# Kernel tuning notes

Hardware: AMD Instinct MI355X
Metric: run time of the kernel (lower is better)

Reference implementation:

```python
import jax, jax.numpy as jnp
import numpy as np

DIM = 768
NUM_EXPERTS = 1536
EXPERT_DIM = 64
NOISE_SCALE = 0.1
B, H, W = 1, 64, 64
N = B * H * W


def setup_inputs() -> dict:
    key = jax.random.key(0)
    ks = jax.random.split(key, 6)
    scaled = lambda k, shape, fan_in: (jax.random.normal(k, shape, jnp.float32) / np.sqrt(fan_in)).astype(jnp.float32)
    return {
        "x": jax.random.normal(ks[0], (B, H, W, DIM), jnp.float32),
        "noise": jax.random.normal(ks[1], (N, NUM_EXPERTS), jnp.float32),
        "gate_w": scaled(ks[2], (NUM_EXPERTS, DIM), DIM),
        "gate_b": jnp.zeros((NUM_EXPERTS,), jnp.float32),
        "expert_w": scaled(ks[3], (NUM_EXPERTS, EXPERT_DIM, DIM), DIM),  # torch Linear weight layout (out, in)
        "expert_b": jnp.zeros((NUM_EXPERTS, EXPERT_DIM), jnp.float32),
        "proj_w": scaled(ks[4], (DIM, EXPERT_DIM), EXPERT_DIM),
        "proj_b": jnp.zeros((DIM,), jnp.float32),
    }


def reference(x, noise, gate_w, gate_b, expert_w, expert_b, proj_w, proj_b):
    orig_shape = x.shape
    xf = x.reshape(-1, orig_shape[-1])  # (N, DIM)
    # Noisy gating
    scores = xf @ gate_w.T + gate_b + noise * NOISE_SCALE  # (N, E)
    gate_weights = jax.nn.softmax(scores, axis=-1)
    top_w, top_i = jax.lax.top_k(gate_weights, 1)  # (N, 1), (N, 1)
    idx = top_i[:, 0]  # (N,)
    # Gather only the selected expert per token (same math as the redundant
    # dense all-expert compute followed by a gather in the original).
    w_sel = expert_w[idx]  # (N, EXPERT_DIM, DIM)
    b_sel = expert_b[idx]  # (N, EXPERT_DIM)
    y = jnp.einsum('nd,nod->no', xf, w_sel) + b_sel  # (N, EXPERT_DIM)
    out_flat = (y @ proj_w.T + proj_b) * top_w  # (N, DIM); top_w broadcasts (N,1)
    return out_flat.reshape(orig_shape)
```

## Files before the change

### kernel.cpp

```cpp
#include <hip/hip_runtime.h>
#include <hip/hip_bf16.h>

#define NT 4096
#define DIM 768
#define NE 1536
#define ED 64
#define GAP_THR 8e-3f

typedef __attribute__((ext_vector_type(8))) short short8v;
typedef __attribute__((ext_vector_type(4))) float f32x4;

__device__ __forceinline__ unsigned short f2bf(float f) {
  unsigned int u = __float_as_uint(f);
  unsigned int r = (u + 0x7fffu + ((u >> 16) & 1u)) >> 16;
  return (unsigned short)r;
}
__device__ __forceinline__ float bf2f(unsigned short h) {
  return __uint_as_float(((unsigned int)h) << 16);
}

__device__ __forceinline__ void gload16(const void* g, void* l) {
  __builtin_amdgcn_global_load_lds((const __attribute__((address_space(1))) void*)g,
                                   (__attribute__((address_space(3))) void*)l, 16, 0, 0);
}

__device__ __forceinline__ void top2_merge(float& m1, int& i1, float& m2, int& i2,
                                           float om1, int oi1, float om2, int oi2) {
  if (om1 > m1 || (om1 == m1 && oi1 < i1)) {
    if (m1 > om2 || (m1 == om2 && i1 < oi2)) { m2 = m1; i2 = i1; }
    else { m2 = om2; i2 = oi2; }
    m1 = om1; i1 = oi1;
  } else {
    if (om1 > m2 || (om1 == m2 && oi1 < i2)) { m2 = om1; i2 = oi1; }
  }
}

__global__ __launch_bounds__(256) void split_all(
    const float* __restrict__ x, const float* __restrict__ gw,
    unsigned short* __restrict__ xhi, unsigned short* __restrict__ xlo,
    unsigned short* __restrict__ ghi, unsigned short* __restrict__ glo,
    int* __restrict__ rc_cnt) {
  if (blockIdx.x == 0 && threadIdx.x == 0) *rc_cnt = 0;
  const int nx4 = NT * DIM / 4;
  const int ng4 = NE * DIM / 4;
  int i = blockIdx.x * 256 + threadIdx.x;
  const float* src; unsigned short* hi; unsigned short* lo; int j;
  if (i < nx4) { src = x; hi = xhi; lo = xlo; j = i; }
  else { j = i - nx4; if (j >= ng4) return; src = gw; hi = ghi; lo = glo; }
  float4 v = ((const float4*)src)[j];
  unsigned short h0 = f2bf(v.x), h1 = f2bf(v.y), h2 = f2bf(v.z), h3 = f2bf(v.w);
  ((ushort4*)hi)[j] = make_ushort4(h0, h1, h2, h3);
  ((ushort4*)lo)[j] = make_ushort4(f2bf(v.x - bf2f(h0)), f2bf(v.y - bf2f(h1)),
                                   f2bf(v.z - bf2f(h2)), f2bf(v.w - bf2f(h3)));
}

__global__ __launch_bounds__(256) void gate_mfma(
    const unsigned short* __restrict__ xhi, const unsigned short* __restrict__ xlo,
    const unsigned short* __restrict__ ghi, const unsigned short* __restrict__ glo,
    const float* __restrict__ gb, const float* __restrict__ noise,
    float4* __restrict__ part_a, int* __restrict__ part_i2) {
  __shared__ __align__(16) unsigned short sA[2 * 128 * 32];
  __shared__ __align__(16) unsigned short sB[2 * 128 * 32];
  const int tid = threadIdx.x;
  const int w = tid >> 6, lane = tid & 63;
  const int wr = w >> 1, wc = w & 1;
  const int bm = blockIdx.x, bn = blockIdx.y;
  const int fr = lane & 15;
  const int fg = lane >> 4;
  const int gsw = fg ^ ((fr >> 1) & 3);

  f32x4 acc[4][4];
#pragma unroll
  for (int i = 0; i < 4; i++)
#pragma unroll
    for (int j = 0; j < 4; j++) acc[i][j] = (f32x4){0.f, 0.f, 0.f, 0.f};

  const size_t arow = (size_t)bm * 128 * DIM;
  const size_t brow = (size_t)bn * 128 * DIM;
  const int sr_lo = tid >> 2;
  const int sg = (tid & 3) ^ ((tid >> 3) & 3);

  for (int kt = 0; kt < DIM; kt += 32) {
    __syncthreads();
#pragma unroll
    for (int h = 0; h < 2; h++) {
      const int r = h * 64 + sr_lo;
      const size_t asrc = arow + (size_t)r * DIM + kt + sg * 8;
      const size_t bsrc = brow + (size_t)r * DIM + kt + sg * 8;
      const int dofs = h * 2048 + w * 512;
      gload16(xhi + asrc, &sA[dofs]);
      gload16(xlo + asrc, &sA[4096 + dofs]);
      gload16(ghi + bsrc, &sB[dofs]);
      gload16(glo + bsrc, &sB[4096 + dofs]);
    }
    __syncthreads();

    short8v ah[4], al[4], bh[4], bl[4];
#pragma unroll
    for (int mf = 0; mf < 4; mf++) {
      int ro = (wr * 64 + mf * 16 + fr) * 32 + gsw * 8;
      ah[mf] = *(const short8v*)&sA[ro];
      al[mf] = *(const short8v*)&sA[4096 + ro];
    }
#pragma unroll
    for (int nf = 0; nf < 4; nf++) {
      int ro = (wc * 64 + nf * 16 + fr) * 32 + gsw * 8;
      bh[nf] = *(const short8v*)&sB[ro];
      bl[nf] = *(const short8v*)&sB[4096 + ro];
    }
#pragma unroll
    for (int mf = 0; mf < 4; mf++)
#pragma unroll
      for (int nf = 0; nf < 4; nf++) {
        f32x4 c = acc[mf][nf];
        c = __builtin_amdgcn_mfma_f32_16x16x32_bf16(ah[mf], bh[nf], c, 0, 0, 0);
        c = __builtin_amdgcn_mfma_f32_16x16x32_bf16(ah[mf], bl[nf], c, 0, 0, 0);
        c = __builtin_amdgcn_mfma_f32_16x16x32_bf16(al[mf], bh[nf], c, 0, 0, 0);
        acc[mf][nf] = c;
      }
  }

  const int gm0 = bm * 128 + wr * 64;
  const int gn0 = bn * 128 + wc * 64;
  const int chunk = bn * 2 + wc;
  int gcol[4]; float gbv[4];
#pragma unroll
  for (int nf = 0; nf < 4; nf++) { gcol[nf] = gn0 + nf * 16 + fr; gbv[nf] = gb[gcol[nf]]; }
#pragma unroll
  for (int mf = 0; mf < 4; mf++) {
    float sv[4][4];
#pragma unroll
    for (int nf = 0; nf < 4; nf++)
#pragma unroll
      for (int reg = 0; reg < 4; reg++) {
        int gm = gm0 + mf * 16 + fg * 4 + reg;
        sv[nf][reg] = acc[mf][nf][reg] + gbv[nf] + 0.1f * noise[(size_t)gm * NE + gcol[nf]];
      }
#pragma unroll
    for (int reg = 0; reg < 4; reg++) {
      float m1 = sv[0][reg]; int i1 = gcol[0];
      float m2 = -3e38f; int i2 = 0x7fffffff;
#pragma unroll
      for (int nf = 1; nf < 4; nf++) {
        float v = sv[nf][reg]; int ii = gcol[nf];
        if (v > m1 || (v == m1 && ii < i1)) { m2 = m1; i2 = i1; m1 = v; i1 = ii; }
        else if (v > m2 || (v == m2 && ii < i2)) { m2 = v; i2 = ii; }
      }
#pragma unroll
      for (int off = 1; off <= 8; off <<= 1) {
        float om1 = __shfl_xor(m1, off, 64); int oi1 = __shfl_xor(i1, off, 64);
        float om2 = __shfl_xor(m2, off, 64); int oi2 = __shfl_xor(i2, off, 64);
        top2_merge(m1, i1, m2, i2, om1, oi1, om2, oi2);
      }
      float ssum = 0.f;
#pragma unroll
      for (int nf = 0; nf < 4; nf++) ssum += __expf(sv[nf][reg] - m1);
#pragma unroll
      for (int off = 1; off <= 8; off <<= 1) ssum += __shfl_xor(ssum, off, 64);
      if (fr == 0) {
        int gm = gm0 + mf * 16 + fg * 4 + reg;
        part_a[(size_t)gm * 24 + chunk] = make_float4(m1, m2, ssum, __int_as_float(i1));
        part_i2[(size_t)gm * 24 + chunk] = i2;
      }
    }
  }
}

__global__ __launch_bounds__(256) void finalize(
    const float4* __restrict__ part_a, const int* __restrict__ part_i2,
    float* __restrict__ topw, int* __restrict__ idx,
    int* __restrict__ rc_count, int* __restrict__ rc_n, int* __restrict__ rc_i2) {
  const int wv = threadIdx.x >> 6, lane = threadIdx.x & 63;
  const int n = blockIdx.x * 4 + wv;
  float m1 = -3e38f, m2 = -3e38f, lm1 = -3e38f, lsum = 0.f;
  int i1 = 0x7fffffff, i2 = 0x7fffffff;
  if (lane < 24) {
    float4 pa = part_a[(size_t)n * 24 + lane];
    m1 = pa.x; m2 = pa.y; lsum = pa.z; i1 = __float_as_int(pa.w);
    i2 = part_i2[(size_t)n * 24 + lane];
    lm1 = pa.x;
  }
#pragma unroll
  for (int off = 1; off <= 32; off <<= 1) {
    float om1 = __shfl_xor(m1, off, 64); int oi1 = __shfl_xor(i1, off, 64);
    float om2 = __shfl_xor(m2, off, 64); int oi2 = __shfl_xor(i2, off, 64);
    top2_merge(m1, i1, m2, i2, om1, oi1, om2, oi2);
  }
  float contrib = (lane < 24) ? __expf(lm1 - m1) * lsum : 0.f;
#pragma unroll
  for (int off = 1; off <= 32; off <<= 1) contrib += __shfl_xor(contrib, off, 64);
  if (lane == 0) {
    topw[n] = 1.0f / contrib;
    idx[n] = i1;
    if (m1 - m2 < GAP_THR) {
      int p = atomicAdd(rc_count, 1);
      rc_n[p] = n; rc_i2[p] = i2;
    }
  }
}

__global__ __launch_bounds__(256) void recheck(
    const float* __restrict__ x, const float* __restrict__ gw,
    const float* __restrict__ gb, const float* __restrict__ noise,
    const int* __restrict__ rc_n, const int* __restrict__ rc_i2,
    const int* __restrict__ rc_count, int* __restrict__ idx) {
  __shared__ float r1[4], r2[4];
  const int cnt = *rc_count;
  const int tid = threadIdx.x;
  const int w = tid >> 6, lane = tid & 63;
  for (int t = blockIdx.x; t < cnt; t += gridDim.x) {
    const int n = rc_n[t];
    const int e1 = idx[n], e2 = rc_i2[t];
    const float* xr = x + (size_t)n * DIM;
    const float* w1 = gw + (size_t)e1 * DIM;
    const float* w2 = gw + (size_t)e2 * DIM;
    float p1 = 0.f, p2 = 0.f;
    for (int k = tid; k < DIM; k += 256) {
      float xv = xr[k];
      p1 += xv * w1[k];
      p2 += xv * w2[k];
    }
#pragma unroll
    for (int off = 32; off; off >>= 1) {
      p1 += __shfl_xor(p1, off, 64);
      p2 += __shfl_xor(p2, off, 64);
    }
    if (lane == 0) { r1[w] = p1; r2[w] = p2; }
    __syncthreads();
    if (tid == 0) {
      float s1 = r1[0] + r1[1] + r1[2] + r1[3] + gb[e1] + 0.1f * noise[(size_t)n * NE + e1];
      float s2 = r2[0] + r2[1] + r2[2] + r2[3] + gb[e2] + 0.1f * noise[(size_t)n * NE + e2];
      if (s2 > s1 || (s2 == s1 && e2 < e1)) idx[n] = e2;
    }
    __syncthreads();
  }
}

__global__ __launch_bounds__(256) void expert_y(
    const float* __restrict__ x, const float* __restrict__ ew,
    const float* __restrict__ eb, const int* __restrict__ idx,
    float* __restrict__ y) {
  const int e = blockIdx.x;
  __shared__ int toklist[128];
  __shared__ int ntok_s;
  __shared__ __align__(16) float Wl[64 * 64];
  __shared__ __align__(16) float xs[8 * DIM];
  const int tid = threadIdx.x;
  const int w = tid >> 6;
  const int lane = tid & 63;
  const int o_sub = lane & 15, d_sub = lane >> 4;
  const int o = w * 16 + o_sub;

  if (tid == 0) ntok_s = 0;
  __syncthreads();
  for (int q = tid; q < NT / 4; q += 256) {
    int4 v = ((const int4*)idx)[q];
    int n0 = q * 4;
    if (v.x == e) { toklist[atomicAdd(&ntok_s, 1) & 127] = n0; }
    if (v.y == e) { toklist[atomicAdd(&ntok_s, 1) & 127] = n0 + 1; }
    if (v.z == e) { toklist[atomicAdd(&ntok_s, 1) & 127] = n0 + 2; }
    if (v.w == e) { toklist[atomicAdd(&ntok_s, 1) & 127] = n0 + 3; }
  }
  __syncthreads();
  const int cnt = min(ntok_s, 128);
  if (cnt == 0) return;

  const float4* W4 = (const float4*)(ew + (size_t)e * ED * DIM);
  const float4* X4 = (const float4*)x;

  for (int c0 = 0; c0 < cnt; c0 += 8) {
    const int cc = min(8, cnt - c0);
    __syncthreads();
    for (int k = 0; k < 6; k++) {
      int f = k * 256 + tid;
      if (f < cc * 192) {
        int t = f / 192, p = f - t * 192;
        gload16(&X4[(size_t)toklist[c0 + t] * 192 + p], &xs[f * 4]);
      }
    }

    float acc[8] = {};
    for (int ch = 0; ch < 12; ch++) {
#pragma unroll
      for (int k = 0; k < 4; k++) {
        int G = k * 256 + tid;
        int ro = G >> 4, g = G & 15;
        gload16(&W4[(size_t)ro * 192 + ch * 16 + (g ^ (ro & 7))], &Wl[G * 4]);
      }
      __syncthreads();

      f32x4 Wr[4];
#pragma unroll
      for (int j = 0; j < 4; j++)
        Wr[j] = *(const f32x4*)&Wl[(o * 16 + ((d_sub * 4 + j) ^ (o & 7))) * 4];
      __syncthreads();

      const int xbase = ch * 64 + d_sub * 16;
#pragma unroll
      for (int t = 0; t < 8; t++) {
        if (t < cc) {
#pragma unroll
          for (int j = 0; j < 4; j++) {
            f32x4 xv = *(const f32x4*)&xs[t * DIM + xbase + j * 4];
            acc[t] += Wr[j].x * xv.x + Wr[j].y * xv.y + Wr[j].z * xv.z + Wr[j].w * xv.w;
          }
        }
      }
    }

    const float ebv = eb[e * ED + w * 16 + o_sub];
#pragma unroll
    for (int t = 0; t < 8; t++) {
      if (t < cc) {
        float r = acc[t];
        r += __shfl_xor(r, 16, 64);
        r += __shfl_xor(r, 32, 64);
        if (lane < 16) y[(size_t)toklist[c0 + t] * ED + w * 16 + o_sub] = r + ebv;
      }
    }
  }
}

__global__ __launch_bounds__(256) void proj_kernel(
    const float* __restrict__ y, const float* __restrict__ pw,
    const float* __restrict__ pb, const float* __restrict__ topw,
    float* __restrict__ out) {
  const int b = blockIdx.x;
  const int tid = threadIdx.x;
  __shared__ float4 ys4[8 * 16];
  __shared__ float tw[8];
  if (tid < 128) {
    int t = tid >> 4, q = tid & 15;
    ys4[tid] = ((const float4*)y)[((size_t)b * 8 + t) * 16 + q];
  }
  if (tid < 8) tw[tid] = topw[b * 8 + tid];
  __syncthreads();
  const float4* pw4 = (const float4*)pw;
#pragma unroll
  for (int c = 0; c < 3; c++) {
    int d = c * 256 + tid;
    float4 pwv[16];
#pragma unroll
    for (int q = 0; q < 16; q++) pwv[q] = pw4[(size_t)d * 16 + q];
    float pbv = pb[d];
    for (int t = 0; t < 8; t++) {
      const float4* yv4 = &ys4[t * 16];
      float s = 0.f;
#pragma unroll
      for (int q = 0; q < 16; q++) {
        float4 yv = yv4[q];
        s += pwv[q].x * yv.x + pwv[q].y * yv.y + pwv[q].z * yv.z + pwv[q].w * yv.w;
      }
      out[((size_t)b * 8 + t) * DIM + d] = (s + pbv) * tw[t];
    }
  }
}

extern "C" void kernel_launch(void* const* d_in, const int* in_sizes, int n_in,
                              void* d_out, int out_size, void* d_ws, size_t ws_size,
                              hipStream_t stream) {
  const float* x      = (const float*)d_in[0];
  const float* noise  = (const float*)d_in[1];
  const float* gate_w = (const float*)d_in[2];
  const float* gate_b = (const float*)d_in[3];
  const float* ew     = (const float*)d_in[4];
  const float* eb     = (const float*)d_in[5];
  const float* pw     = (const float*)d_in[6];
  const float* pb     = (const float*)d_in[7];
  float* out = (float*)d_out;

  char* ws = (char*)d_ws;
  unsigned short* xhi    = (unsigned short*)(ws);
  unsigned short* xlo    = (unsigned short*)(ws + 6291456);
  unsigned short* ghi    = (unsigned short*)(ws + 12582912);
  unsigned short* glo    = (unsigned short*)(ws + 14942208);
  float4*         part_a = (float4*)(ws + 17301504);
  int*            part_i2= (int*)  (ws + 18874368);
  float*          y      = (float*)(ws + 19267584);
  float*          topw   = (float*)(ws + 20316160);
  int*            idx    = (int*)  (ws + 20332544);
  int*            rc_cnt = (int*)  (ws + 20348928);
  int*            rc_n   = (int*)  (ws + 20349184);
  int*            rc_i2  = (int*)  (ws + 20365568);

  split_all<<<(NT * DIM / 4 + NE * DIM / 4 + 255) / 256, 256, 0, stream>>>(
      x, gate_w, xhi, xlo, ghi, glo, rc_cnt);
  gate_mfma<<<dim3(NT / 128, NE / 128), 256, 0, stream>>>(
      xhi, xlo, ghi, glo, gate_b, noise, part_a, part_i2);
  finalize<<<NT / 4, 256, 0, stream>>>(part_a, part_i2, topw, idx,
                                       rc_cnt, rc_n, rc_i2);
  recheck<<<32, 256, 0, stream>>>(x, gate_w, gate_b, noise, rc_n, rc_i2, rc_cnt, idx);
  expert_y<<<NE, 256, 0, stream>>>(x, ew, eb, idx, y);
  proj_kernel<<<NT / 8, 256, 0, stream>>>(y, pw, pb, topw, out);
}
```

Before: 218.9 us.

## Double-buffer expert weight chunks in LDS and widen recheck grid

```diff
diff --git a/kernel.cpp b/kernel.cpp
--- a/kernel.cpp
+++ b/kernel.cpp
@@ -243,11 +243,10 @@
   const int e = blockIdx.x;
   __shared__ int toklist[128];
   __shared__ int ntok_s;
-  __shared__ __align__(16) float Wl[64 * 64];
+  __shared__ __align__(16) float Wl[2][64 * 32];
   __shared__ __align__(16) float xs[8 * DIM];
   const int tid = threadIdx.x;
-  const int w = tid >> 6;
-  const int lane = tid & 63;
+  const int w = tid >> 6, lane = tid & 63;
   const int o_sub = lane & 15, d_sub = lane >> 4;
   const int o = w * 16 + o_sub;
 
@@ -256,10 +255,10 @@
   for (int q = tid; q < NT / 4; q += 256) {
     int4 v = ((const int4*)idx)[q];
     int n0 = q * 4;
-    if (v.x == e) { toklist[atomicAdd(&ntok_s, 1) & 127] = n0; }
-    if (v.y == e) { toklist[atomicAdd(&ntok_s, 1) & 127] = n0 + 1; }
-    if (v.z == e) { toklist[atomicAdd(&ntok_s, 1) & 127] = n0 + 2; }
-    if (v.w == e) { toklist[atomicAdd(&ntok_s, 1) & 127] = n0 + 3; }
+    if (v.x == e) toklist[atomicAdd(&ntok_s, 1) & 127] = n0;
+    if (v.y == e) toklist[atomicAdd(&ntok_s, 1) & 127] = n0 + 1;
+    if (v.z == e) toklist[atomicAdd(&ntok_s, 1) & 127] = n0 + 2;
+    if (v.w == e) toklist[atomicAdd(&ntok_s, 1) & 127] = n0 + 3;
   }
   __syncthreads();
   const int cnt = min(ntok_s, 128);
@@ -267,10 +266,18 @@
 
   const float4* W4 = (const float4*)(ew + (size_t)e * ED * DIM);
   const float4* X4 = (const float4*)x;
+  const int ro0 = tid >> 3;
+  const int ro1 = (256 + tid) >> 3;
+  const int g0 = (tid & 7) ^ (ro0 & 7);
+  const int g1 = (tid & 7) ^ (ro1 & 7);
+  const int rg0 = (o * 8 + ((d_sub * 2 + 0) ^ (o & 7))) * 4;
+  const int rg1 = (o * 8 + ((d_sub * 2 + 1) ^ (o & 7))) * 4;
+  const float ebv = eb[e * ED + o];
 
   for (int c0 = 0; c0 < cnt; c0 += 8) {
     const int cc = min(8, cnt - c0);
     __syncthreads();
+#pragma unroll
     for (int k = 0; k < 6; k++) {
       int f = k * 256 + tid;
       if (f < cc * 192) {
@@ -278,44 +285,47 @@
         gload16(&X4[(size_t)toklist[c0 + t] * 192 + p], &xs[f * 4]);
       }
     }
+    gload16(&W4[(size_t)ro0 * 192 + g0], &Wl[0][tid * 4]);
+    gload16(&W4[(size_t)ro1 * 192 + g1], &Wl[0][(256 + tid) * 4]);
+    asm volatile("s_waitcnt vmcnt(0)" ::: "memory");
+    __builtin_amdgcn_s_barrier();
 
     float acc[8] = {};
-    for (int ch = 0; ch < 12; ch++) {
-#pragma unroll
-      for (int k = 0; k < 4; k++) {
-        int G = k * 256 + tid;
-        int ro = G >> 4, g = G & 15;
-        gload16(&W4[(size_t)ro * 192 + ch * 16 + (g ^ (ro & 7))], &Wl[G * 4]);
-      }
-      __syncthreads();
-
-      f32x4 Wr[4];
-#pragma unroll
-      for (int j = 0; j < 4; j++)
-        Wr[j] = *(const f32x4*)&Wl[(o * 16 + ((d_sub * 4 + j) ^ (o & 7))) * 4];
-      __syncthreads();
-
-      const int xbase = ch * 64 + d_sub * 16;
+    for (int ch = 0; ch < 24; ch++) {
+      const int cur = ch & 1;
+      if (ch < 23) {
+        const int nxt = cur ^ 1;
+        gload16(&W4[(size_t)ro0 * 192 + (ch + 1) * 8 + g0], &Wl[nxt][tid * 4]);
+        gload16(&W4[(size_t)ro1 * 192 + (ch + 1) * 8 + g1], &Wl[nxt][(256 + tid) * 4]);
+        asm volatile("s_waitcnt vmcnt(2)" ::: "memory");
+      } else {
+        asm volatile("s_waitcnt vmcnt(0)" ::: "memory");
+      }
+      __builtin_amdgcn_s_barrier();
+      asm volatile("" ::: "memory");
+      f32x4 w0 = *(const f32x4*)&Wl[cur][rg0];
+      f32x4 w1 = *(const f32x4*)&Wl[cur][rg1];
+      const int xb = ch * 32 + d_sub * 8;
 #pragma unroll
       for (int t = 0; t < 8; t++) {
         if (t < cc) {
-#pragma unroll
-          for (int j = 0; j < 4; j++) {
-            f32x4 xv = *(const f32x4*)&xs[t * DIM + xbase + j * 4];
-            acc[t] += Wr[j].x * xv.x + Wr[j].y * xv.y + Wr[j].z * xv.z + Wr[j].w * xv.w;
-          }
+          f32x4 xa = *(const f32x4*)&xs[t * DIM + xb];
+          f32x4 xc = *(const f32x4*)&xs[t * DIM + xb + 4];
+          acc[t] += w0.x * xa.x + w0.y * xa.y + w0.z * xa.z + w0.w * xa.w
+                  + w1.x * xc.x + w1.y * xc.y + w1.z * xc.z + w1.w * xc.w;
         }
       }
-    }
-
-    const float ebv = eb[e * ED + w * 16 + o_sub];
+      asm volatile("" ::: "memory");
+      __builtin_amdgcn_s_barrier();
+    }
+
 #pragma unroll
     for (int t = 0; t < 8; t++) {
       if (t < cc) {
         float r = acc[t];
         r += __shfl_xor(r, 16, 64);
         r += __shfl_xor(r, 32, 64);
-        if (lane < 16) y[(size_t)toklist[c0 + t] * ED + w * 16 + o_sub] = r + ebv;
+        if (lane < 16) y[(size_t)toklist[c0 + t] * ED + o] = r + ebv;
       }
     }
   }
@@ -389,7 +399,7 @@
       xhi, xlo, ghi, glo, gate_b, noise, part_a, part_i2);
   finalize<<<NT / 4, 256, 0, stream>>>(part_a, part_i2, topw, idx,
                                        rc_cnt, rc_n, rc_i2);
-  recheck<<<32, 256, 0, stream>>>(x, gate_w, gate_b, noise, rc_n, rc_i2, rc_cnt, idx);
+  recheck<<<64, 256, 0, stream>>>(x, gate_w, gate_b, noise, rc_n, rc_i2, rc_cnt, idx);
   expert_y<<<NE, 256, 0, stream>>>(x, ew, eb, idx, y);
   proj_kernel<<<NT / 8, 256, 0, stream>>>(y, pw, pb, topw, out);
 }
```

New measurement: 227.7 us. 1.04x slower.

## Read expert weights directly into registers, reduce partial sums through LDS

Applied to the files above, without the earlier changes.

```diff
diff --git a/kernel.cpp b/kernel.cpp
--- a/kernel.cpp
+++ b/kernel.cpp
@@ -243,23 +243,20 @@
   const int e = blockIdx.x;
   __shared__ int toklist[128];
   __shared__ int ntok_s;
-  __shared__ __align__(16) float Wl[64 * 64];
-  __shared__ __align__(16) float xs[8 * DIM];
+  __shared__ __align__(16) float xs[8][DIM];
+  __shared__ __align__(16) float part[4][8][64];
   const int tid = threadIdx.x;
-  const int w = tid >> 6;
-  const int lane = tid & 63;
-  const int o_sub = lane & 15, d_sub = lane >> 4;
-  const int o = w * 16 + o_sub;
+  const int w = tid >> 6, lane = tid & 63;
 
   if (tid == 0) ntok_s = 0;
   __syncthreads();
   for (int q = tid; q < NT / 4; q += 256) {
     int4 v = ((const int4*)idx)[q];
     int n0 = q * 4;
-    if (v.x == e) { toklist[atomicAdd(&ntok_s, 1) & 127] = n0; }
-    if (v.y == e) { toklist[atomicAdd(&ntok_s, 1) & 127] = n0 + 1; }
-    if (v.z == e) { toklist[atomicAdd(&ntok_s, 1) & 127] = n0 + 2; }
-    if (v.w == e) { toklist[atomicAdd(&ntok_s, 1) & 127] = n0 + 3; }
+    if (v.x == e) toklist[atomicAdd(&ntok_s, 1) & 127] = n0;
+    if (v.y == e) toklist[atomicAdd(&ntok_s, 1) & 127] = n0 + 1;
+    if (v.z == e) toklist[atomicAdd(&ntok_s, 1) & 127] = n0 + 2;
+    if (v.w == e) toklist[atomicAdd(&ntok_s, 1) & 127] = n0 + 3;
   }
   __syncthreads();
   const int cnt = min(ntok_s, 128);
@@ -267,56 +264,37 @@
 
   const float4* W4 = (const float4*)(ew + (size_t)e * ED * DIM);
   const float4* X4 = (const float4*)x;
+  const size_t wbase = (size_t)lane * 192 + w * 48;
 
   for (int c0 = 0; c0 < cnt; c0 += 8) {
     const int cc = min(8, cnt - c0);
     __syncthreads();
-    for (int k = 0; k < 6; k++) {
-      int f = k * 256 + tid;
-      if (f < cc * 192) {
-        int t = f / 192, p = f - t * 192;
-        gload16(&X4[(size_t)toklist[c0 + t] * 192 + p], &xs[f * 4]);
-      }
-    }
-
-    float acc[8] = {};
-    for (int ch = 0; ch < 12; ch++) {
-#pragma unroll
-      for (int k = 0; k < 4; k++) {
-        int G = k * 256 + tid;
-        int ro = G >> 4, g = G & 15;
-        gload16(&W4[(size_t)ro * 192 + ch * 16 + (g ^ (ro & 7))], &Wl[G * 4]);
-      }
-      __syncthreads();
-
-      f32x4 Wr[4];
-#pragma unroll
-      for (int j = 0; j < 4; j++)
-        Wr[j] = *(const f32x4*)&Wl[(o * 16 + ((d_sub * 4 + j) ^ (o & 7))) * 4];
-      __syncthreads();
-
-      const int xbase = ch * 64 + d_sub * 16;
+    for (int f = tid; f < cc * 192; f += 256) {
+      int t = f / 192, p = f - t * 192;
+      *(float4*)&xs[t][p * 4] = X4[(size_t)toklist[c0 + t] * 192 + p];
+    }
+    __syncthreads();
+
+    float acc[8] = {0.f, 0.f, 0.f, 0.f, 0.f, 0.f, 0.f, 0.f};
+#pragma unroll 4
+    for (int j = 0; j < 48; j++) {
+      float4 wv = W4[wbase + j];
+      const int d = (w * 48 + j) * 4;
 #pragma unroll
       for (int t = 0; t < 8; t++) {
         if (t < cc) {
-#pragma unroll
-          for (int j = 0; j < 4; j++) {
-            f32x4 xv = *(const f32x4*)&xs[t * DIM + xbase + j * 4];
-            acc[t] += Wr[j].x * xv.x + Wr[j].y * xv.y + Wr[j].z * xv.z + Wr[j].w * xv.w;
-          }
+          float4 xv = *(const float4*)&xs[t][d];
+          acc[t] += wv.x * xv.x + wv.y * xv.y + wv.z * xv.z + wv.w * xv.w;
         }
       }
     }
-
-    const float ebv = eb[e * ED + w * 16 + o_sub];
-#pragma unroll
-    for (int t = 0; t < 8; t++) {
-      if (t < cc) {
-        float r = acc[t];
-        r += __shfl_xor(r, 16, 64);
-        r += __shfl_xor(r, 32, 64);
-        if (lane < 16) y[(size_t)toklist[c0 + t] * ED + w * 16 + o_sub] = r + ebv;
-      }
+#pragma unroll
+    for (int t = 0; t < 8; t++) part[w][t][lane] = acc[t];
+    __syncthreads();
+    for (int p = tid; p < cc * 64; p += 256) {
+      int t = p >> 6, oo = p & 63;
+      float r = part[0][t][oo] + part[1][t][oo] + part[2][t][oo] + part[3][t][oo];
+      y[(size_t)toklist[c0 + t] * ED + oo] = r + eb[e * ED + oo];
     }
   }
 }
@@ -389,7 +367,7 @@
       xhi, xlo, ghi, glo, gate_b, noise, part_a, part_i2);
   finalize<<<NT / 4, 256, 0, stream>>>(part_a, part_i2, topw, idx,
                                        rc_cnt, rc_n, rc_i2);
-  recheck<<<32, 256, 0, stream>>>(x, gate_w, gate_b, noise, rc_n, rc_i2, rc_cnt, idx);
+  recheck<<<64, 256, 0, stream>>>(x, gate_w, gate_b, noise, rc_n, rc_i2, rc_cnt, idx);
   expert_y<<<NE, 256, 0, stream>>>(x, ew, eb, idx, y);
   proj_kernel<<<NT / 8, 256, 0, stream>>>(y, pw, pb, topw, out);
 }
```

Measured after the change: 308.7 us. 41.0% more time.
